# Kernel tuning notes

Hardware: AMD Instinct MI355X
Metric: run time of the kernel (lower is better)

Reference implementation:

```python
import jax, jax.numpy as jnp
import numpy as np

EPS = 1e-5
GN_GROUPS_DIV = 4  # nn.GroupNorm(out_ch // 4, out_ch)


def conv1x1(x, w, b=None):
    # x [B,C,H,W], w [O,C]
    y = jnp.einsum('bchw,oc->bohw', x, w)
    return y if b is None else y + b[None, :, None, None]


def conv2d(x, w, pad):
    return jax.lax.conv_general_dilated(
        x, w, (1, 1), [(pad, pad), (pad, pad)],
        dimension_numbers=('NCHW', 'OIHW', 'NCHW'))


def batchnorm(x, gamma, beta):
    # training-mode BatchNorm2d: batch statistics over (B,H,W)
    mu = jnp.mean(x, axis=(0, 2, 3), keepdims=True)
    var = jnp.var(x, axis=(0, 2, 3), keepdims=True)
    xn = (x - mu) * jax.lax.rsqrt(var + EPS)
    return xn * gamma[None, :, None, None] + beta[None, :, None, None]


def groupnorm(x, gamma, beta, groups):
    B, C, H, W = x.shape
    xg = x.reshape(B, groups, C // groups, H, W)
    mu = jnp.mean(xg, axis=(2, 3, 4), keepdims=True)
    var = jnp.var(xg, axis=(2, 3, 4), keepdims=True)
    xn = ((xg - mu) * jax.lax.rsqrt(var + EPS)).reshape(B, C, H, W)
    return xn * gamma[None, :, None, None] + beta[None, :, None, None]


def bilinear_sample(img, ys, xs):
    # Faithful to DSC._bilinear_interpolate_3D: floor/floor+1 coords are
    # clamped BEFORE computing weights, so samples exactly at the last
    # row/col get all-zero weights (output zeroed there), as in torch.
    H, W = img.shape[2], img.shape[3]
    y0 = jnp.floor(ys)
    x0 = jnp.floor(xs)
    y0c = jnp.clip(y0, 0, H - 1).astype(jnp.int32)
    y1c = jnp.clip(y0 + 1, 0, H - 1).astype(jnp.int32)
    x0c = jnp.clip(x0, 0, W - 1).astype(jnp.int32)
    x1c = jnp.clip(x0 + 1, 0, W - 1).astype(jnp.int32)
    y0f, y1f = y0c.astype(ys.dtype), y1c.astype(ys.dtype)
    x0f, x1f = x0c.astype(xs.dtype), x1c.astype(xs.dtype)
    w00 = (y1f - ys) * (x1f - xs)
    w01 = (y1f - ys) * (xs - x0f)
    w10 = (ys - y0f) * (x1f - xs)
    w11 = (ys - y0f) * (xs - x0f)
    g = lambda yy, xx: img[:, :, yy, xx]  # irregular gather, [B,C,H,W]
    return (g(y0c, x0c) * w00 + g(y0c, x1c) * w01 +
            g(y1c, x0c) * w10 + g(y1c, x1c) * w11)


def _forward(x, ca_w1, ca_w2, sa_w, gate_w, off_w, off_b, off_gamma, off_beta,
             dsc_w, dsc_b, gn_gamma, gn_beta, bn_gamma, bn_beta, prelu_a,
             out_w, out_b):
    B, C, H, W = x.shape
    res = x

    # --- ChannelAttention2D (CBAM): shared MLP on avg & max pooled desc ---
    avg = jnp.mean(x, axis=(2, 3), keepdims=True)          # [B,C,1,1]
    mx = jnp.max(x, axis=(2, 3), keepdims=True)
    mlp = lambda v: conv1x1(jax.nn.relu(conv1x1(v, ca_w1)), ca_w2)
    ca = jax.nn.sigmoid(mlp(avg) + mlp(mx))
    x_ca = x * ca

    # --- SpatialAttention2D (CBAM): 7x7 conv over [mean,max] channel maps ---
    s_avg = jnp.mean(x, axis=1, keepdims=True)
    s_max = jnp.max(x, axis=1, keepdims=True)
    sa = jax.nn.sigmoid(conv2d(jnp.concatenate([s_avg, s_max], axis=1), sa_w, pad=3))
    x_sa = x * sa

    # --- gate fuse ---
    fuse = x_sa + x_ca
    guide = jax.nn.sigmoid(conv1x1(fuse, gate_w))
    xg = x * guide

    # --- DSConv(kernel_size=1, morph=0, if_offset=True) ---
    # offset branch (computed as in torch; with num_points=1 the iterative
    # offset accumulation zeroes the center point, so offsets do NOT move
    # the sampling grid -> zero gradient flows to the offset conv)
    off = jnp.tanh(batchnorm(conv2d(xg, off_w, pad=1) + off_b[None, :, None, None],
                             off_gamma, off_beta))
    del off  # dead in fwd math for kernel_size=1 (faithful to source)

    ii = jnp.arange(H, dtype=x.dtype)[:, None] * jnp.ones((1, W), x.dtype)
    jj = jnp.ones((H, 1), x.dtype) * jnp.arange(W, dtype=x.dtype)[None, :]
    deformed = bilinear_sample(xg, ii, jj)  # identity gather except last row/col zeroed

    d = conv1x1(deformed, dsc_w, dsc_b)     # dsc_conv_x with (k,1)=(1,1) kernel
    d = groupnorm(d, gn_gamma, gn_beta, C // GN_GROUPS_DIV)
    d = jax.nn.relu(d)

    # --- residual + BN + PReLU + 1x1 out conv ---
    y = d + res
    y = batchnorm(y, bn_gamma, bn_beta)
    a = prelu_a.reshape(())
    y = jnp.where(y >= 0, y, a * y)
    return conv1x1(y, out_w, out_b)         # [B,1,H,W]


def setup_inputs() -> dict:
    key = jax.random.key(0)
    ks = jax.random.split(key, 12)
    B, C, H, W = 8, 64, 256, 256
    r = C // 16  # CBAM ratio 16
    f32 = jnp.float32
    n = lambda k, shp, s: (jax.random.normal(k, shp, dtype=f32) * s)
    return {
        'x': n(ks[0], (B, C, H, W), 1.0),
        'ca_w1': n(ks[1], (r, C), 0.1),
        'ca_w2': n(ks[2], (C, r), 0.1),
        'sa_w': n(ks[3], (1, 2, 7, 7), 0.1),
        'gate_w': n(ks[4], (C, C), 0.05),
        'off_w': n(ks[5], (2, C, 3, 3), 0.05),
        'off_b': jnp.zeros((2,), f32),
        'off_gamma': jnp.ones((2,), f32),
        'off_beta': jnp.zeros((2,), f32),
        'dsc_w': n(ks[6], (C, C), 0.05),
        'dsc_b': jnp.zeros((C,), f32),
        'gn_gamma': jnp.ones((C,), f32),
        'gn_beta': jnp.zeros((C,), f32),
        'bn_gamma': jnp.ones((C,), f32),
        'bn_beta': jnp.zeros((C,), f32),
        'prelu_a': jnp.full((1,), 0.25, f32),
        'out_w': n(ks[7], (1, C), 0.1),
        'out_b': jnp.zeros((1,), f32),
    }


def reference(x, ca_w1, ca_w2, sa_w, gate_w, off_w, off_b, off_gamma, off_beta,
              dsc_w, dsc_b, gn_gamma, gn_beta, bn_gamma, bn_beta, prelu_a,
              out_w, out_b):
    return _forward(x, ca_w1, ca_w2, sa_w, gate_w, off_w, off_b, off_gamma,
                    off_beta, dsc_w, dsc_b, gn_gamma, gn_beta, bn_gamma,
                    bn_beta, prelu_a, out_w, out_b)
```

## Files before the change

kernel.cpp:

```cpp
#include <hip/hip_runtime.h>

#define HW 65536
#define CB 64
#define NB 8

typedef __attribute__((ext_vector_type(4))) float f32x4;
typedef __attribute__((ext_vector_type(8))) short s16x8;

__device__ __forceinline__ float sigm(float v) { return 1.f / (1.f + __expf(-v)); }

__device__ __forceinline__ unsigned encf(float f) {
    unsigned u = __float_as_uint(f);
    return (u & 0x80000000u) ? ~u : (u | 0x80000000u);
}
__device__ __forceinline__ float decf(unsigned u) {
    return (u & 0x80000000u) ? __uint_as_float(u & 0x7fffffffu) : __uint_as_float(~u);
}
__device__ __forceinline__ unsigned f2bf(float f) {
    unsigned u = __float_as_uint(f);
    u += 0x7fffu + ((u >> 16) & 1u);
    return u >> 16;
}
__device__ __forceinline__ float bf2f(unsigned h) {
    return __uint_as_float(h << 16);
}
__device__ __forceinline__ int swz(int row, int w) { return (row << 5) + (w ^ ((row & 7) << 2)); }

__global__ __launch_bounds__(256) void k_pre(
    const float* __restrict__ x, unsigned short* __restrict__ xpc,
    float* __restrict__ pool_scr, unsigned* __restrict__ pmax_scr,
    unsigned* __restrict__ sm)
{
    __shared__ unsigned tile[8192];
    __shared__ float scrS[8][64];
    __shared__ float scrM[8][64];
    const int t = threadIdx.x;
    const int b = blockIdx.x >> 8;
    const int pbase = (blockIdx.x & 255) << 8;
    const size_t xb = ((size_t)(b << 6)) * HW + pbase + t;
    const int s = (t & 7) << 2;

    float psum = 0.f, pmax = -1e30f;
    #pragma unroll
    for (int cg = 0; cg < 4; ++cg) {
        float v[16];
        #pragma unroll
        for (int k = 0; k < 16; ++k)
            v[k] = x[xb + (size_t)((cg << 4) + k) * HW];
        #pragma unroll
        for (int k = 0; k < 16; ++k) { psum += v[k]; pmax = fmaxf(pmax, v[k]); }
        unsigned w[8];
        #pragma unroll
        for (int k = 0; k < 8; ++k) w[k] = f2bf(v[2 * k]) | (f2bf(v[2 * k + 1]) << 16);
        *(uint4*)&tile[(t << 5) + (((cg << 3)) ^ s)]     = make_uint4(w[0], w[1], w[2], w[3]);
        *(uint4*)&tile[(t << 5) + (((cg << 3) + 4) ^ s)] = make_uint4(w[4], w[5], w[6], w[7]);
    }
    sm[(size_t)b * HW + pbase + t] = f2bf(psum * (1.f / 64.f)) | (f2bf(pmax) << 16);
    __syncthreads();

    {
        const int cp = t & 31, q = t >> 5;
        float s0 = 0.f, s1 = 0.f, m0 = -1e30f, m1 = -1e30f;
        #pragma unroll 8
        for (int i = 0; i < 32; ++i) {
            const int px = (q << 5) + i;
            const unsigned u = tile[(px << 5) + (cp ^ ((px & 7) << 2))];
            const float a0 = bf2f(u & 0xffffu), a1 = bf2f(u >> 16);
            s0 += a0; s1 += a1;
            m0 = fmaxf(m0, a0); m1 = fmaxf(m1, a1);
        }
        scrS[q][2 * cp] = s0; scrS[q][2 * cp + 1] = s1;
        scrM[q][2 * cp] = m0; scrM[q][2 * cp + 1] = m1;
    }
    {
        unsigned short* xp = xpc + (((size_t)b * HW + pbase) << 6);
        #pragma unroll
        for (int k = 0; k < 8; ++k) {
            const int px = (k << 5) + (t >> 3);
            const int w = ((t & 7) << 2) ^ ((px & 7) << 2);
            const uint4 v = *(const uint4*)&tile[(px << 5) + w];
            *(uint4*)(xp + (k << 11) + (t << 3)) = v;
        }
    }
    __syncthreads();
    if (t < 64) {
        float ss = 0.f, mm = -1e30f;
        #pragma unroll
        for (int q = 0; q < 8; ++q) { ss += scrS[q][t]; mm = fmaxf(mm, scrM[q][t]); }
        const int copy = blockIdx.x & 7;
        atomicAdd(&pool_scr[(((b << 3) + copy) << 6) + t], ss);
        atomicMax(&pmax_scr[(((b << 3) + copy) << 6) + t], encf(mm));
    }
}

__global__ __launch_bounds__(256) void k_sa_ca(
    const unsigned* __restrict__ sm, const float* __restrict__ w,
    const float* __restrict__ pool_scr, const unsigned* __restrict__ pmax_scr,
    const float* __restrict__ w1, const float* __restrict__ w2,
    unsigned short* __restrict__ sa, float* __restrict__ ca)
{
    const int t = threadIdx.x;
    const int b = blockIdx.x >> 8;
    const int pix = ((blockIdx.x & 255) << 8) | t;
    const int i = pix >> 8, j = pix & 255;
    const unsigned* src = sm + (size_t)b * HW;
    float acc = 0.f;
    #pragma unroll
    for (int ki = 0; ki < 7; ++ki) {
        const int y = i + ki - 3;
        if ((unsigned)y < 256u) {
            #pragma unroll
            for (int kj = 0; kj < 7; ++kj) {
                const int xx = j + kj - 3;
                if ((unsigned)xx < 256u) {
                    const unsigned u = src[(y << 8) | xx];
                    acc += bf2f(u & 0xffffu) * w[ki * 7 + kj] +
                           bf2f(u >> 16)     * w[49 + ki * 7 + kj];
                }
            }
        }
    }
    sa[(size_t)b * HW + pix] = (unsigned short)f2bf(sigm(acc));

    if ((blockIdx.x & 255) == 0) {
        __shared__ float av[CB], mv[CB], hh[8];
        if (t < CB) {
            float ss = 0.f; unsigned mm = 0u;
            #pragma unroll
            for (int r = 0; r < 8; ++r) {
                ss += pool_scr[(((b << 3) + r) << 6) + t];
                mm = max(mm, pmax_scr[(((b << 3) + r) << 6) + t]);
            }
            av[t] = ss * (1.f / (float)HW);
            mv[t] = decf(mm);
        }
        __syncthreads();
        if (t < 8) {
            const int h = t & 3;
            const float* v = (t < 4) ? av : mv;
            float ssum = 0;
            for (int c = 0; c < CB; ++c) ssum += w1[h * CB + c] * v[c];
            hh[t] = fmaxf(ssum, 0.f);
        }
        __syncthreads();
        if (t < CB) {
            float ssum = 0;
            #pragma unroll
            for (int h = 0; h < 4; ++h) ssum += w2[t * 4 + h] * (hh[h] + hh[4 + h]);
            ca[b * CB + t] = sigm(ssum);
        }
    }
}

__global__ __launch_bounds__(256, 3) void k_main(
    const unsigned short* __restrict__ xpc, const unsigned short* __restrict__ sa,
    const float* __restrict__ ca, const float* __restrict__ gw,
    const float* __restrict__ dw, const float* __restrict__ db,
    unsigned short* __restrict__ dbuf, float* __restrict__ gn_sum,
    float* __restrict__ gn_sq)
{
    __shared__ unsigned lds[12320];
    __shared__ float saL[128];
    __shared__ float caL[64];
    const int t = threadIdx.x;
    const int wv = t >> 6, l = t & 63, hi = l >> 4, lo = l & 15;
    const int b = blockIdx.x >> 9;
    const int pbase = (blockIdx.x & 511) << 7;

    {
        const int orow = t >> 2, cq = (t & 3) << 4;
        const float* gsrc = gw + (orow << 6) + cq;
        const float* dsrc = dw + (orow << 6) + cq;
        unsigned ug[8], ud[8];
        #pragma unroll
        for (int j = 0; j < 8; ++j) {
            ug[j] = f2bf(gsrc[2 * j]) | (f2bf(gsrc[2 * j + 1]) << 16);
            ud[j] = f2bf(dsrc[2 * j]) | (f2bf(dsrc[2 * j + 1]) << 16);
        }
        const int wbase = (t & 3) << 3;
        *(uint4*)&lds[swz(orow, wbase)]            = make_uint4(ug[0], ug[1], ug[2], ug[3]);
        *(uint4*)&lds[swz(orow, wbase + 4)]        = make_uint4(ug[4], ug[5], ug[6], ug[7]);
        *(uint4*)&lds[2048 + swz(orow, wbase)]     = make_uint4(ud[0], ud[1], ud[2], ud[3]);
        *(uint4*)&lds[2048 + swz(orow, wbase + 4)] = make_uint4(ud[4], ud[5], ud[6], ud[7]);
    }
    if (t < 128) saL[t] = bf2f(sa[(size_t)b * HW + pbase + t]);
    else if (t < 192) caL[t - 128] = ca[(b << 6) + (t - 128)];

    {
        const unsigned short* xp = xpc + (((size_t)b * HW + pbase) << 6);
        #pragma unroll
        for (int k = 0; k < 4; ++k) {
            const int idx = (k << 8) + t;
            const int px = idx >> 3;
            const int wg = (idx & 7) << 2;
            const uint4 v = *(const uint4*)(xp + (idx << 3));
            *(uint4*)&lds[8192 + (px << 5) + (wg ^ ((px & 7) << 2))] = v;
        }
    }
    __syncthreads();

    {
        const int wb2 = (wv << 3) + (hi << 1);
        const int cbb = wb2 << 1;
        const float c0 = caL[cbb], c1 = caL[cbb + 1], c2 = caL[cbb + 2], c3 = caL[cbb + 3];
        #pragma unroll
        for (int n = 0; n < 8; ++n) {
            const int pxl = (n << 4) + lo;
            const float sv = saL[pxl];
            const uint2 xv = *(const uint2*)&lds[8192 + swz(pxl, wb2)];
            uint2 o;
            o.x = f2bf(bf2f(xv.x & 0xffffu) * (sv + c0)) | (f2bf(bf2f(xv.x >> 16) * (sv + c1)) << 16);
            o.y = f2bf(bf2f(xv.y & 0xffffu) * (sv + c2)) | (f2bf(bf2f(xv.y >> 16) * (sv + c3)) << 16);
            *(uint2*)&lds[4096 + swz(pxl, wb2)] = o;
        }
    }
    __syncthreads();

    f32x4 acc[8];
    #pragma unroll
    for (int n = 0; n < 8; ++n) acc[n] = (f32x4){0.f, 0.f, 0.f, 0.f};
    {
        const int arow = (wv << 4) + lo;
        const s16x8 a0 = __builtin_bit_cast(s16x8, *(const uint4*)&lds[swz(arow, hi << 2)]);
        const s16x8 a1 = __builtin_bit_cast(s16x8, *(const uint4*)&lds[swz(arow, (hi << 2) + 16)]);
        #pragma unroll
        for (int n = 0; n < 8; ++n) {
            const int brow = (n << 4) + lo;
            const s16x8 b0 = __builtin_bit_cast(s16x8, *(const uint4*)&lds[4096 + swz(brow, hi << 2)]);
            const s16x8 b1 = __builtin_bit_cast(s16x8, *(const uint4*)&lds[4096 + swz(brow, (hi << 2) + 16)]);
            acc[n] = __builtin_amdgcn_mfma_f32_16x16x32_bf16(a0, b0, acc[n], 0, 0, 0);
            acc[n] = __builtin_amdgcn_mfma_f32_16x16x32_bf16(a1, b1, acc[n], 0, 0, 0);
        }
    }
    __syncthreads();

    {
        const bool row255 = (pbase >> 8) == 255;
        const bool halfblk = (pbase & 128) != 0;
        const int wb2 = (wv << 3) + (hi << 1);
        #pragma unroll
        for (int n = 0; n < 8; ++n) {
            const int pxl = (n << 4) + lo;
            const uint2 xv = *(const uint2*)&lds[8192 + swz(pxl, wb2)];
            const bool zero = row255 || (halfblk && pxl == 127);
            float xg0 = zero ? 0.f : bf2f(xv.x & 0xffffu) * sigm(acc[n][0]);
            float xg1 = zero ? 0.f : bf2f(xv.x >> 16)     * sigm(acc[n][1]);
            float xg2 = zero ? 0.f : bf2f(xv.y & 0xffffu) * sigm(acc[n][2]);
            float xg3 = zero ? 0.f : bf2f(xv.y >> 16)     * sigm(acc[n][3]);
            uint2 o;
            o.x = f2bf(xg0) | (f2bf(xg1) << 16);
            o.y = f2bf(xg2) | (f2bf(xg3) << 16);
            *(uint2*)&lds[4096 + swz(pxl, wb2)] = o;
        }
    }
    __syncthreads();

    f32x4 acc2[8];
    #pragma unroll
    for (int n = 0; n < 8; ++n) acc2[n] = (f32x4){0.f, 0.f, 0.f, 0.f};
    {
        const int arow = (wv << 4) + lo;
        const s16x8 a0 = __builtin_bit_cast(s16x8, *(const uint4*)&lds[2048 + swz(arow, hi << 2)]);
        const s16x8 a1 = __builtin_bit_cast(s16x8, *(const uint4*)&lds[2048 + swz(arow, (hi << 2) + 16)]);
        #pragma unroll
        for (int n = 0; n < 8; ++n) {
            const int brow = (n << 4) + lo;
            const s16x8 b0 = __builtin_bit_cast(s16x8, *(const uint4*)&lds[4096 + swz(brow, hi << 2)]);
            const s16x8 b1 = __builtin_bit_cast(s16x8, *(const uint4*)&lds[4096 + swz(brow, (hi << 2) + 16)]);
            acc2[n] = __builtin_amdgcn_mfma_f32_16x16x32_bf16(a0, b0, acc2[n], 0, 0, 0);
            acc2[n] = __builtin_amdgcn_mfma_f32_16x16x32_bf16(a1, b1, acc2[n], 0, 0, 0);
        }
    }

    float gs = 0.f, gq = 0.f;
    {
        const float4 bv = *(const float4*)(db + (wv << 4) + (hi << 2));
        unsigned short* dp = dbuf + (((size_t)b * HW + pbase) << 6) + (wv << 4) + (hi << 2);
        #pragma unroll
        for (int n = 0; n < 8; ++n) {
            const int pxl = (n << 4) + lo;
            const float d0 = acc2[n][0] + bv.x, d1 = acc2[n][1] + bv.y;
            const float d2 = acc2[n][2] + bv.z, d3 = acc2[n][3] + bv.w;
            gs += d0 + d1 + d2 + d3;
            gq += d0 * d0 + d1 * d1 + d2 * d2 + d3 * d3;
            uint2 o;
            o.x = f2bf(d0) | (f2bf(d1) << 16);
            o.y = f2bf(d2) | (f2bf(d3) << 16);
            *(uint2*)(dp + ((size_t)pxl << 6)) = o;
        }
    }
    #pragma unroll
    for (int o = 1; o < 16; o <<= 1) { gs += __shfl_xor(gs, o); gq += __shfl_xor(gq, o); }
    float* smf = (float*)&lds[12288];
    if (lo == 0) { smf[(((wv << 2) + hi) << 1)] = gs; smf[(((wv << 2) + hi) << 1) + 1] = gq; }
    __syncthreads();
    if (t < 16) {
        atomicAdd(&gn_sum[(b << 4) + t], smf[2 * t]);
        atomicAdd(&gn_sq[(b << 4) + t],  smf[2 * t + 1]);
    }
}

__global__ __launch_bounds__(256) void k_gnbn(
    const unsigned short* __restrict__ xpc, unsigned short* __restrict__ dy,
    const float* __restrict__ gn_sum, const float* __restrict__ gn_sq,
    const float* __restrict__ gamma, const float* __restrict__ beta,
    float* __restrict__ bn_scr)
{
    const int t = threadIdx.x;
    const size_t P0 = (size_t)blockIdx.x << 8;
    const int b = (int)(P0 >> 16);
    __shared__ float ga[CB], gb[CB];
    __shared__ float red[4][128];
    if (t < CB) {
        const int g = t >> 2;
        const float n4 = 4.f * (float)HW;
        const float mu = gn_sum[b * 16 + g] / n4;
        const float var = gn_sq[b * 16 + g] / n4 - mu * mu;
        const float a = rsqrtf(var + 1e-5f) * gamma[t];
        ga[t] = a; gb[t] = beta[t] - mu * a;
    }
    __syncthreads();
    const int o8 = (t & 7) << 3;
    float ar[8], br[8];
    #pragma unroll
    for (int k = 0; k < 8; ++k) { ar[k] = ga[o8 + k]; br[k] = gb[o8 + k]; }
    float as[8], aq[8];
    #pragma unroll
    for (int k = 0; k < 8; ++k) { as[k] = 0.f; aq[k] = 0.f; }
    for (int i = 0; i < 8; ++i) {
        const size_t P = P0 + (i << 5) + (t >> 3);
        const size_t idx = (P << 6) + o8;
        const uint4 dv = *(const uint4*)(dy + idx);
        const uint4 xv = *(const uint4*)(xpc + idx);
        const unsigned dw_[4] = {dv.x, dv.y, dv.z, dv.w};
        const unsigned xw_[4] = {xv.x, xv.y, xv.z, xv.w};
        uint4 o;
        unsigned ow_[4];
        #pragma unroll
        for (int p = 0; p < 4; ++p) {
            const int k0 = 2 * p;
            const float y0 = fmaxf(bf2f(dw_[p] & 0xffffu) * ar[k0] + br[k0], 0.f) + bf2f(xw_[p] & 0xffffu);
            const float y1 = fmaxf(bf2f(dw_[p] >> 16) * ar[k0 + 1] + br[k0 + 1], 0.f) + bf2f(xw_[p] >> 16);
            as[k0] += y0; aq[k0] += y0 * y0;
            as[k0 + 1] += y1; aq[k0 + 1] += y1 * y1;
            ow_[p] = f2bf(y0) | (f2bf(y1) << 16);
        }
        o.x = ow_[0]; o.y = ow_[1]; o.z = ow_[2]; o.w = ow_[3];
        *(uint4*)(dy + idx) = o;
    }
    #pragma unroll
    for (int k = 0; k < 8; ++k) {
        #pragma unroll
        for (int m = 8; m < 64; m <<= 1) {
            as[k] += __shfl_xor(as[k], m);
            aq[k] += __shfl_xor(aq[k], m);
        }
    }
    if ((t & 63) < 8) {
        const int o = t & 7, wvv = t >> 6;
        #pragma unroll
        for (int k = 0; k < 8; ++k) {
            red[wvv][o * 16 + k] = as[k];
            red[wvv][o * 16 + 8 + k] = aq[k];
        }
    }
    __syncthreads();
    if (t < 128) {
        const int o = t >> 4, st = (t >> 3) & 1, k = t & 7;
        const float v = red[0][t] + red[1][t] + red[2][t] + red[3][t];
        atomicAdd(&bn_scr[(blockIdx.x & 7) * 128 + st * 64 + o * 8 + k], v);
    }
}

__global__ __launch_bounds__(256) void k_out(
    const unsigned short* __restrict__ y, const float* __restrict__ bn_scr,
    const float* __restrict__ gamma, const float* __restrict__ beta,
    const float* __restrict__ pa, const float* __restrict__ ow,
    const float* __restrict__ ob, float* __restrict__ out)
{
    const int t = threadIdx.x;
    __shared__ float A[CB], Bs[CB], W[CB];
    if (t < CB) {
        float s = 0.f, q = 0.f;
        #pragma unroll
        for (int r = 0; r < 8; ++r) { s += bn_scr[r * 128 + t]; q += bn_scr[r * 128 + 64 + t]; }
        const float n = (float)NB * (float)HW;
        const float mu = s / n;
        const float var = q / n - mu * mu;
        const float a = rsqrtf(var + 1e-5f) * gamma[t];
        A[t] = a; Bs[t] = beta[t] - mu * a; W[t] = ow[t];
    }
    __syncthreads();
    const size_t P = ((size_t)blockIdx.x << 8) + t;
    const unsigned short* yp = y + (P << 6);
    const float alpha = pa[0];
    float acc = ob[0];
    #pragma unroll
    for (int q = 0; q < 8; ++q) {
        const uint4 v = *(const uint4*)(yp + (q << 3));
        const unsigned vw[4] = {v.x, v.y, v.z, v.w};
        #pragma unroll
        for (int p = 0; p < 4; ++p) {
            const int c = (q << 3) + 2 * p;
            float z0 = bf2f(vw[p] & 0xffffu) * A[c] + Bs[c];
            float z1 = bf2f(vw[p] >> 16) * A[c + 1] + Bs[c + 1];
            z0 = z0 >= 0.f ? z0 : alpha * z0;
            z1 = z1 >= 0.f ? z1 : alpha * z1;
            acc += W[c] * z0 + W[c + 1] * z1;
        }
    }
    out[P] = acc;
}

extern "C" void kernel_launch(void* const* d_in, const int* in_sizes, int n_in,
                              void* d_out, int out_size, void* d_ws, size_t ws_size,
                              hipStream_t stream)
{
    const float* x        = (const float*)d_in[0];
    const float* ca_w1    = (const float*)d_in[1];
    const float* ca_w2    = (const float*)d_in[2];
    const float* sa_w     = (const float*)d_in[3];
    const float* gate_w   = (const float*)d_in[4];
    const float* dsc_w    = (const float*)d_in[9];
    const float* dsc_b    = (const float*)d_in[10];
    const float* gn_gamma = (const float*)d_in[11];
    const float* gn_beta  = (const float*)d_in[12];
    const float* bn_gamma = (const float*)d_in[13];
    const float* bn_beta  = (const float*)d_in[14];
    const float* prelu_a  = (const float*)d_in[15];
    const float* out_w    = (const float*)d_in[16];
    const float* out_b    = (const float*)d_in[17];
    float* out = (float*)d_out;

    char* ws = (char*)d_ws;
    size_t off = 0;
    auto alloc = [&](size_t bytes) -> char* {
        char* p = ws + off;
        off = (off + bytes + 255) & ~(size_t)255;
        return p;
    };
    unsigned short* dbuf = (unsigned short*)alloc((size_t)NB * HW * CB * 2);
    unsigned short* xpc  = (unsigned short*)alloc((size_t)NB * HW * CB * 2);
    unsigned* smb        = (unsigned*)alloc((size_t)NB * HW * 4);
    unsigned short* sab  = (unsigned short*)alloc((size_t)NB * HW * 2);
    float* cav   = (float*)alloc(512 * 4);
    char* stats  = alloc(9472 * 4);
    float*    pool_scr = (float*)stats;
    unsigned* pmax_scr = (unsigned*)(stats + 4096 * 4);
    float*    gn_sum   = (float*)(stats + 8192 * 4);
    float*    gn_sq    = (float*)(stats + 8320 * 4);
    float*    bn_scr   = (float*)(stats + 8448 * 4);
    (void)in_sizes; (void)n_in; (void)out_size; (void)ws_size;

    hipMemsetAsync(stats, 0, 9472 * 4, stream);

    k_pre  <<<NB * 256, 256, 0, stream>>>(x, xpc, pool_scr, pmax_scr, smb);
    k_sa_ca<<<NB * 256, 256, 0, stream>>>(smb, sa_w, pool_scr, pmax_scr,
                                          ca_w1, ca_w2, sab, cav);
    k_main <<<NB * 512, 256, 0, stream>>>(xpc, sab, cav, gate_w, dsc_w, dsc_b,
                                          dbuf, gn_sum, gn_sq);
    k_gnbn <<<2048,     256, 0, stream>>>(xpc, dbuf, gn_sum, gn_sq, gn_gamma, gn_beta, bn_scr);
    k_out  <<<2048,     256, 0, stream>>>(dbuf, bn_scr, bn_gamma, bn_beta,
                                          prelu_a, out_w, out_b, out);
}
```

Measured before the change: 167.7 us.

## Fuse spatial and channel attention into main kernel; precompute bf16 weights once

The separate spatial/channel-attention kernel is removed. Each main-kernel block now computes the 7x7 spatial-attention conv for its 128 pixels and the small channel-attention MLP itself. A new tiny init kernel converts the gate and DSC weights to swizzled bf16 once and zeroes the stats buffer, replacing the memset. This removes a launch plus the sa/ca global round trip and the per-block weight conversion, at the cost of redundant channel-MLP work in every block and extra syncs and latency before the main GEMM.

```diff
diff --git a/kernel.cpp b/kernel.cpp
--- a/kernel.cpp
+++ b/kernel.cpp
@@ -25,6 +25,33 @@
     return __uint_as_float(h << 16);
 }
 __device__ __forceinline__ int swz(int row, int w) { return (row << 5) + (w ^ ((row & 7) << 2)); }
+
+__global__ __launch_bounds__(256) void k_init(
+    const float* __restrict__ gw, const float* __restrict__ dw,
+    unsigned* __restrict__ wbuf, unsigned* __restrict__ stats)
+{
+    const int t = threadIdx.x;
+    if (blockIdx.x < 2) {
+        const float* src = (blockIdx.x == 0) ? gw : dw;
+        unsigned* dst = wbuf + (blockIdx.x << 11);
+        const int orow = t >> 2, cq = (t & 3) << 4;
+        const float* s = src + (orow << 6) + cq;
+        unsigned u[8];
+        #pragma unroll
+        for (int j = 0; j < 8; ++j)
+            u[j] = f2bf(s[2 * j]) | (f2bf(s[2 * j + 1]) << 16);
+        const int wbase = (t & 3) << 3;
+        *(uint4*)&dst[swz(orow, wbase)]     = make_uint4(u[0], u[1], u[2], u[3]);
+        *(uint4*)&dst[swz(orow, wbase + 4)] = make_uint4(u[4], u[5], u[6], u[7]);
+    } else {
+        const int base = (blockIdx.x - 2) * 4736;
+        #pragma unroll
+        for (int k = 0; k < 19; ++k) {
+            const int idx = base + k * 256 + t;
+            if (idx < base + 4736 && idx < 9472) stats[idx] = 0u;
+        }
+    }
+}
 
 __global__ __launch_bounds__(256) void k_pre(
     const float* __restrict__ x, unsigned short* __restrict__ xpc,
@@ -93,99 +120,29 @@
     }
 }
 
-__global__ __launch_bounds__(256) void k_sa_ca(
-    const unsigned* __restrict__ sm, const float* __restrict__ w,
+__global__ __launch_bounds__(256, 3) void k_main(
+    const unsigned short* __restrict__ xpc, const unsigned* __restrict__ smb,
+    const float* __restrict__ saw,
     const float* __restrict__ pool_scr, const unsigned* __restrict__ pmax_scr,
     const float* __restrict__ w1, const float* __restrict__ w2,
-    unsigned short* __restrict__ sa, float* __restrict__ ca)
-{
-    const int t = threadIdx.x;
-    const int b = blockIdx.x >> 8;
-    const int pix = ((blockIdx.x & 255) << 8) | t;
-    const int i = pix >> 8, j = pix & 255;
-    const unsigned* src = sm + (size_t)b * HW;
-    float acc = 0.f;
-    #pragma unroll
-    for (int ki = 0; ki < 7; ++ki) {
-        const int y = i + ki - 3;
-        if ((unsigned)y < 256u) {
-            #pragma unroll
-            for (int kj = 0; kj < 7; ++kj) {
-                const int xx = j + kj - 3;
-                if ((unsigned)xx < 256u) {
-                    const unsigned u = src[(y << 8) | xx];
-                    acc += bf2f(u & 0xffffu) * w[ki * 7 + kj] +
-                           bf2f(u >> 16)     * w[49 + ki * 7 + kj];
-                }
-            }
-        }
-    }
-    sa[(size_t)b * HW + pix] = (unsigned short)f2bf(sigm(acc));
-
-    if ((blockIdx.x & 255) == 0) {
-        __shared__ float av[CB], mv[CB], hh[8];
-        if (t < CB) {
-            float ss = 0.f; unsigned mm = 0u;
-            #pragma unroll
-            for (int r = 0; r < 8; ++r) {
-                ss += pool_scr[(((b << 3) + r) << 6) + t];
-                mm = max(mm, pmax_scr[(((b << 3) + r) << 6) + t]);
-            }
-            av[t] = ss * (1.f / (float)HW);
-            mv[t] = decf(mm);
-        }
-        __syncthreads();
-        if (t < 8) {
-            const int h = t & 3;
-            const float* v = (t < 4) ? av : mv;
-            float ssum = 0;
-            for (int c = 0; c < CB; ++c) ssum += w1[h * CB + c] * v[c];
-            hh[t] = fmaxf(ssum, 0.f);
-        }
-        __syncthreads();
-        if (t < CB) {
-            float ssum = 0;
-            #pragma unroll
-            for (int h = 0; h < 4; ++h) ssum += w2[t * 4 + h] * (hh[h] + hh[4 + h]);
-            ca[b * CB + t] = sigm(ssum);
-        }
-    }
-}
-
-__global__ __launch_bounds__(256, 3) void k_main(
-    const unsigned short* __restrict__ xpc, const unsigned short* __restrict__ sa,
-    const float* __restrict__ ca, const float* __restrict__ gw,
-    const float* __restrict__ dw, const float* __restrict__ db,
+    const unsigned* __restrict__ wbuf, const float* __restrict__ db,
     unsigned short* __restrict__ dbuf, float* __restrict__ gn_sum,
     float* __restrict__ gn_sq)
 {
     __shared__ unsigned lds[12320];
     __shared__ float saL[128];
     __shared__ float caL[64];
+    __shared__ float caA[64], caM[64], hh[8];
     const int t = threadIdx.x;
     const int wv = t >> 6, l = t & 63, hi = l >> 4, lo = l & 15;
     const int b = blockIdx.x >> 9;
     const int pbase = (blockIdx.x & 511) << 7;
 
-    {
-        const int orow = t >> 2, cq = (t & 3) << 4;
-        const float* gsrc = gw + (orow << 6) + cq;
-        const float* dsrc = dw + (orow << 6) + cq;
-        unsigned ug[8], ud[8];
-        #pragma unroll
-        for (int j = 0; j < 8; ++j) {
-            ug[j] = f2bf(gsrc[2 * j]) | (f2bf(gsrc[2 * j + 1]) << 16);
-            ud[j] = f2bf(dsrc[2 * j]) | (f2bf(dsrc[2 * j + 1]) << 16);
-        }
-        const int wbase = (t & 3) << 3;
-        *(uint4*)&lds[swz(orow, wbase)]            = make_uint4(ug[0], ug[1], ug[2], ug[3]);
-        *(uint4*)&lds[swz(orow, wbase + 4)]        = make_uint4(ug[4], ug[5], ug[6], ug[7]);
-        *(uint4*)&lds[2048 + swz(orow, wbase)]     = make_uint4(ud[0], ud[1], ud[2], ud[3]);
-        *(uint4*)&lds[2048 + swz(orow, wbase + 4)] = make_uint4(ud[4], ud[5], ud[6], ud[7]);
-    }
-    if (t < 128) saL[t] = bf2f(sa[(size_t)b * HW + pbase + t]);
-    else if (t < 192) caL[t - 128] = ca[(b << 6) + (t - 128)];
-
+    #pragma unroll
+    for (int k = 0; k < 4; ++k) {
+        const int idx = (k << 8) + t;
+        *(uint4*)&lds[idx << 2] = *(const uint4*)&wbuf[idx << 2];
+    }
     {
         const unsigned short* xp = xpc + (((size_t)b * HW + pbase) << 6);
         #pragma unroll
@@ -196,6 +153,55 @@
             const uint4 v = *(const uint4*)(xp + (idx << 3));
             *(uint4*)&lds[8192 + (px << 5) + (wg ^ ((px & 7) << 2))] = v;
         }
+    }
+    if (t < 64) {
+        float ss = 0.f; unsigned mm = 0u;
+        #pragma unroll
+        for (int r = 0; r < 8; ++r) {
+            ss += pool_scr[(((b << 3) + r) << 6) + t];
+            mm = max(mm, pmax_scr[(((b << 3) + r) << 6) + t]);
+        }
+        caA[t] = ss * (1.f / (float)HW);
+        caM[t] = decf(mm);
+    }
+    float sav = 0.f;
+    if (t < 128) {
+        const int pix = pbase + t;
+        const int i = pix >> 8, j = pix & 255;
+        const unsigned* src = smb + (size_t)b * HW;
+        float accv = 0.f;
+        #pragma unroll
+        for (int ki = 0; ki < 7; ++ki) {
+            const int y = i + ki - 3;
+            if ((unsigned)y < 256u) {
+                #pragma unroll
+                for (int kj = 0; kj < 7; ++kj) {
+                    const int xx = j + kj - 3;
+                    if ((unsigned)xx < 256u) {
+                        const unsigned u = src[(y << 8) | xx];
+                        accv += bf2f(u & 0xffffu) * saw[ki * 7 + kj] +
+                                bf2f(u >> 16)     * saw[49 + ki * 7 + kj];
+                    }
+                }
+            }
+        }
+        sav = sigm(accv);
+    }
+    __syncthreads();
+    if (t < 8) {
+        const int h = t & 3;
+        const float* v = (t < 4) ? caA : caM;
+        float ssum = 0.f;
+        for (int c = 0; c < CB; ++c) ssum += w1[h * CB + c] * v[c];
+        hh[t] = fmaxf(ssum, 0.f);
+    }
+    __syncthreads();
+    if (t < 128) saL[t] = sav;
+    if (t < 64) {
+        float ssum = 0.f;
+        #pragma unroll
+        for (int h = 0; h < 4; ++h) ssum += w2[t * 4 + h] * (hh[h] + hh[4 + h]);
+        caL[t] = sigm(ssum);
     }
     __syncthreads();
 
@@ -442,8 +448,7 @@
     unsigned short* dbuf = (unsigned short*)alloc((size_t)NB * HW * CB * 2);
     unsigned short* xpc  = (unsigned short*)alloc((size_t)NB * HW * CB * 2);
     unsigned* smb        = (unsigned*)alloc((size_t)NB * HW * 4);
-    unsigned short* sab  = (unsigned short*)alloc((size_t)NB * HW * 2);
-    float* cav   = (float*)alloc(512 * 4);
+    unsigned* wbuf       = (unsigned*)alloc(4096 * 4);
     char* stats  = alloc(9472 * 4);
     float*    pool_scr = (float*)stats;
     unsigned* pmax_scr = (unsigned*)(stats + 4096 * 4);
@@ -452,12 +457,10 @@
     float*    bn_scr   = (float*)(stats + 8448 * 4);
     (void)in_sizes; (void)n_in; (void)out_size; (void)ws_size;
 
-    hipMemsetAsync(stats, 0, 9472 * 4, stream);
-
+    k_init <<<4,        256, 0, stream>>>(gate_w, dsc_w, wbuf, (unsigned*)stats);
     k_pre  <<<NB * 256, 256, 0, stream>>>(x, xpc, pool_scr, pmax_scr, smb);
-    k_sa_ca<<<NB * 256, 256, 0, stream>>>(smb, sa_w, pool_scr, pmax_scr,
-                                          ca_w1, ca_w2, sab, cav);
-    k_main <<<NB * 512, 256, 0, stream>>>(xpc, sab, cav, gate_w, dsc_w, dsc_b,
+    k_main <<<NB * 512, 256, 0, stream>>>(xpc, smb, sa_w, pool_scr, pmax_scr,
+                                          ca_w1, ca_w2, wbuf, dsc_b,
                                           dbuf, gn_sum, gn_sq);
     k_gnbn <<<2048,     256, 0, stream>>>(xpc, dbuf, gn_sum, gn_sq, gn_gamma, gn_beta, bn_scr);
     k_out  <<<2048,     256, 0, stream>>>(dbuf, bn_scr, bn_gamma, bn_beta,
```

New measurement: 201.8 us. 1.2x slower.
